# Optimization experiments

Hardware: AMD Instinct MI355X
Metric: run time of the kernel (lower is better)

The kernel has to match this reference:

```python
import jax, jax.numpy as jnp
import numpy as np

EMB = 1024
HID = 2048
HEADS = 16
CONV = 4


def causal_conv1d(z, w):
    # z: [B, H, T], w: [H, K] depthwise causal conv
    K = w.shape[1]
    T = z.shape[-1]
    zp = jnp.pad(z, ((0, 0), (0, 0), (K - 1, 0)))  # [B, H, T+K-1]
    out = jnp.zeros_like(z)
    for k in range(K):  # tiny fixed loop over taps (K<=4)
        out = out + w[None, :, k, None] * jax.lax.dynamic_slice_in_dim(zp, k, T, axis=2)
    return out


def linear_scan(a, b):
    # h_t = a_t * h_{t-1} + b_t along last axis; associative scan
    def combine(c1, c2):
        a1, b1 = c1
        a2, b2 = c2
        return a1 * a2, a2 * b1 + b2
    _, h = jax.lax.associative_scan(combine, (a, b), axis=-1)
    return h


def setup_inputs() -> dict:
    key = jax.random.key(0)
    k1, k2, k3, k4 = jax.random.split(key, 4)
    x = jax.random.normal(k1, (4, 2048, EMB), dtype=jnp.float32)
    w1 = jax.random.normal(k2, (3 * HID, EMB), dtype=jnp.float32) * (EMB ** -0.5)
    w2 = jax.random.normal(k3, (EMB, HID), dtype=jnp.float32) * (HID ** -0.5)
    conv_weight = jax.random.normal(k4, (HID, CONV), dtype=jnp.float32) * (CONV ** -0.5)
    return {"x": x, "w1": w1, "w2": w2, "conv_weight": conv_weight}


def reference(x, w1, w2, conv_weight):
    bsz, seq_len, _ = x.shape
    head_dim = HID // HEADS
    y = jnp.einsum("bse,he->bsh", x, w1)  # [B, S, 3*HID]
    out1, z, h = jnp.split(y, 3, axis=-1)
    z = jnp.swapaxes(z, 1, 2)  # [B, HID, S]
    h = jnp.swapaxes(h, 1, 2)
    z = causal_conv1d(z, conv_weight)
    z = jax.nn.sigmoid(z)
    z = z.reshape(bsz * HEADS, head_dim, seq_len)
    h = h.reshape(bsz * HEADS, head_dim, seq_len)
    h = linear_scan(1.0 - z, z * h)
    out2 = jnp.swapaxes(h.reshape(bsz, HID, seq_len), 1, 2)  # [B, S, HID]
    out = jax.nn.silu(out1) * out2
    return jnp.einsum("bsh,eh->bse", out, w2)
```

## Files before the change

### kernel.cpp

```cpp
#include <hip/hip_runtime.h>
#include <cstdint>

#define EMB 1024
#define HID 2048
#define BATCH 4
#define SEQ 2048
#define MROWS (BATCH * SEQ)
#define N1 (3 * HID)
#define K1 EMB
#define N2 EMB
#define K2 HID

#define NX (MROWS * EMB)
#define NW1 (N1 * K1)
#define NW2 (N2 * K2)

#define SEG 64
#define SLEN (SEQ / SEG)

typedef unsigned short ushort_t;
typedef __bf16 bf16x8 __attribute__((ext_vector_type(8)));
typedef float f32x4 __attribute__((ext_vector_type(4)));
typedef ushort_t us4 __attribute__((ext_vector_type(4)));

__device__ __forceinline__ ushort_t f2bf(float f) {
    uint32_t u = __builtin_bit_cast(uint32_t, f);
    u += 0x7fffu + ((u >> 16) & 1u);
    return (ushort_t)(u >> 16);
}
__device__ __forceinline__ float bf2f(ushort_t h) {
    uint32_t u = ((uint32_t)h) << 16;
    return __builtin_bit_cast(float, u);
}
__device__ __forceinline__ float bflo(uint32_t v) {
    return __builtin_bit_cast(float, v << 16);
}
__device__ __forceinline__ float bfhi(uint32_t v) {
    return __builtin_bit_cast(float, v & 0xffff0000u);
}
__device__ __forceinline__ float sigm(float x) {
    return 1.f / (1.f + __expf(-x));
}

__device__ __forceinline__ void gload_lds16(const ushort_t* g, const ushort_t* l) {
    __builtin_amdgcn_global_load_lds(
        (const __attribute__((address_space(1))) void*)(uintptr_t)(g),
        (__attribute__((address_space(3))) void*)(uint32_t)(uintptr_t)(l),
        16, 0, 0);
}

__global__ __launch_bounds__(256) void cvt_kernel(
    const float* __restrict__ x, const float* __restrict__ w1,
    const float* __restrict__ w2, ushort_t* __restrict__ xb,
    ushort_t* __restrict__ w1b, ushort_t* __restrict__ w2b) {
    const int i = (blockIdx.x * 256 + threadIdx.x) * 4;
    const float* s;
    ushort_t* d;
    if (i < NX) {
        s = x + i; d = xb + i;
    } else if (i < NX + NW1) {
        s = w1 + (i - NX); d = w1b + (i - NX);
    } else {
        s = w2 + (i - NX - NW1); d = w2b + (i - NX - NW1);
    }
    const float4 v = *(const float4*)s;
    us4 o;
    o.x = f2bf(v.x); o.y = f2bf(v.y); o.z = f2bf(v.z); o.w = f2bf(v.w);
    *(us4*)d = o;
}

__device__ __forceinline__ void lda4(bf16x8 (&af)[2][4], const ushort_t* c,
                                     int arow, int quad, int sw) {
#pragma unroll
    for (int s = 0; s < 2; ++s)
#pragma unroll
        for (int i = 0; i < 4; ++i)
            af[s][i] = *(const bf16x8*)&c[(arow + i * 16) * 64 +
                                          (((s * 4 + quad) ^ sw) << 3)];
}
__device__ __forceinline__ void ldb2(bf16x8 (&bfr)[2][2], const ushort_t* c,
                                     int bcol, int quad, int sw) {
#pragma unroll
    for (int s = 0; s < 2; ++s)
#pragma unroll
        for (int j = 0; j < 2; ++j)
            bfr[s][j] = *(const bf16x8*)&c[(bcol + j * 16) * 64 +
                                           (((s * 4 + quad) ^ sw) << 3)];
}
template <int QM, int QN>
__device__ __forceinline__ void mm16(f32x4 (&acc)[8][4],
                                     const bf16x8 (&af)[2][4],
                                     const bf16x8 (&bfr)[2][2]) {
#pragma unroll
    for (int s = 0; s < 2; ++s)
#pragma unroll
        for (int i = 0; i < 4; ++i)
#pragma unroll
            for (int j = 0; j < 2; ++j)
                acc[QM * 4 + i][QN * 2 + j] =
                    __builtin_amdgcn_mfma_f32_16x16x32_bf16(
                        af[s][i], bfr[s][j], acc[QM * 4 + i][QN * 2 + j], 0, 0, 0);
}

template <bool OUT_BF16>
__global__ __launch_bounds__(512, 2) void gemm256(
    const ushort_t* __restrict__ A, const ushort_t* __restrict__ B,
    void* __restrict__ Cv, int M, int N, int K) {
    __shared__ __align__(16) ushort_t sA[2][2][8192];
    __shared__ __align__(16) ushort_t sB[2][2][8192];

    const int tid  = threadIdx.x;
    const int lane = tid & 63;
    const int wave = tid >> 6;
    const int wm   = wave >> 2;
    const int wn   = wave & 3;
    const int quad = lane >> 4;
    const int l15  = lane & 15;
    const int sw   = lane & 7;

    int wg = blockIdx.x;
    const int nwg = gridDim.x;
    if ((nwg & 7) == 0) wg = (wg & 7) * (nwg >> 3) + (wg >> 3);
    const int nbx = N >> 8;
    const int bx = wg % nbx;
    const int by = wg / nbx;
    const long tm0 = (long)by << 8;
    const long tn0 = (long)bx << 8;

    const ushort_t* gA = A + (size_t)tm0 * K;
    const ushort_t* gB = B + (size_t)tn0 * K;

    const int l8 = lane >> 3;
    const int ss = (lane & 7) ^ l8;
    const uint32_t rA = (uint32_t)((wave & 3) * 16 + l8 + (wave >> 2) * 128);
    const int cB = wave * 16 + l8;
    const uint32_t rB = (uint32_t)((cB >> 5) * 64 + (cB & 31));
    const uint32_t offA0 = rA * (uint32_t)K + (uint32_t)ss * 8u;
    const uint32_t offA1 = offA0 + 8u * (uint32_t)K;
    const uint32_t offB0 = rB * (uint32_t)K + (uint32_t)ss * 8u;
    const uint32_t offB1 = offB0 + 8u * (uint32_t)K;

    const auto stA = [&](int tt, int q) {
        ushort_t* d = &sA[tt & 1][q][wave << 10];
        const size_t ko = (size_t)tt * 64 + (size_t)q * 64 * (size_t)K;
        gload_lds16(gA + ko + offA0, d);
        gload_lds16(gA + ko + offA1, d + 512);
    };
    const auto stB = [&](int tt, int q) {
        ushort_t* d = &sB[tt & 1][q][wave << 10];
        const size_t ko = (size_t)tt * 64 + (size_t)q * 32 * (size_t)K;
        gload_lds16(gB + ko + offB0, d);
        gload_lds16(gB + ko + offB1, d + 512);
    };

    const int arow = wm * 64 + l15;
    const int bcol = wn * 32 + l15;

    f32x4 acc[8][4] = {};
    bf16x8 af0[2][4], af1[2][4], bf0[2][2], bf1[2][2];

    const int NT = K >> 6;

    stA(0, 0); stB(0, 0); stB(0, 1); stA(0, 1);
    asm volatile("s_waitcnt vmcnt(0)" ::: "memory");
    __builtin_amdgcn_s_barrier();

    for (int T = 0; T < NT; ++T) {
        const int cur = T & 1;
        const ushort_t* a0 = &sA[cur][0][0];
        const ushort_t* a1 = &sA[cur][1][0];
        const ushort_t* b0 = &sB[cur][0][0];
        const ushort_t* b1 = &sB[cur][1][0];
        const bool st1 = (T + 1 < NT);

        lda4(af0, a0, arow, quad, sw);
        ldb2(bf0, b0, bcol, quad, sw);
        ldb2(bf1, b1, bcol, quad, sw);
        lda4(af1, a1, arow, quad, sw);
        if (st1) {
            stA(T + 1, 0); stB(T + 1, 0);
            stB(T + 1, 1); stA(T + 1, 1);
        }
        __builtin_amdgcn_s_setprio(1);
        mm16<0, 0>(acc, af0, bf0);
        mm16<0, 1>(acc, af0, bf1);
        mm16<1, 0>(acc, af1, bf0);
        mm16<1, 1>(acc, af1, bf1);
        __builtin_amdgcn_s_setprio(0);
        if (st1) asm volatile("s_waitcnt vmcnt(0)" ::: "memory");
        __builtin_amdgcn_s_barrier();
    }

#pragma unroll
    for (int ai = 0; ai < 8; ++ai) {
        const long row0 = tm0 + wm * 128 + (ai >> 2) * 64 + (ai & 3) * 16 + quad * 4;
#pragma unroll
        for (int bj = 0; bj < 4; ++bj) {
            const long col = tn0 + wn * 64 + (bj >> 1) * 32 + (bj & 1) * 16 + l15;
#pragma unroll
            for (int r = 0; r < 4; ++r) {
                if constexpr (OUT_BF16) {
                    ((ushort_t*)Cv)[(size_t)(row0 + r) * N + col] = f2bf(acc[ai][bj][r]);
                } else {
                    ((float*)Cv)[(size_t)(row0 + r) * N + col] = acc[ai][bj][r];
                }
            }
        }
    }
}

__global__ __launch_bounds__(512, 1) void gemm_mn(
    const ushort_t* __restrict__ A, const ushort_t* __restrict__ B,
    float* __restrict__ C, int M, int N, int K) {
    __shared__ __align__(16) ushort_t sA[3][2][8192];
    __shared__ __align__(16) ushort_t sB[3][8192];

    const int tid  = threadIdx.x;
    const int lane = tid & 63;
    const int wave = tid >> 6;
    const int wm   = wave >> 1;
    const int wn   = wave & 1;
    const int quad = lane >> 4;
    const int l15  = lane & 15;
    const int sw   = lane & 7;

    int wg = blockIdx.x;
    const int nwg = gridDim.x;
    if ((nwg & 7) == 0) wg = (wg & 7) * (nwg >> 3) + (wg >> 3);
    const int nbx = N >> 7;
    const int bx = wg % nbx;
    const int by = wg / nbx;
    const long tm0 = (long)by << 8;
    const long tn0 = (long)bx << 7;

    const ushort_t* gA = A + (size_t)tm0 * K;
    const ushort_t* gB = B + (size_t)tn0 * K;

    const int l8 = lane >> 3;
    const int ss = (lane & 7) ^ l8;
    const uint32_t rA = (uint32_t)((wave & 3) * 16 + l8 + (wave >> 2) * 128);
    const uint32_t rB = (uint32_t)(wave * 16 + l8);
    const uint32_t offA0 = rA * (uint32_t)K + (uint32_t)ss * 8u;
    const uint32_t offA1 = offA0 + 8u * (uint32_t)K;
    const uint32_t offB0 = rB * (uint32_t)K + (uint32_t)ss * 8u;
    const uint32_t offB1 = offB0 + 8u * (uint32_t)K;

    const auto stA = [&](int tt, int q) {
        ushort_t* d = &sA[tt % 3][q][wave << 10];
        const size_t ko = (size_t)tt * 64 + (size_t)q * 64 * (size_t)K;
        gload_lds16(gA + ko + offA0, d);
        gload_lds16(gA + ko + offA1, d + 512);
    };
    const auto stB = [&](int tt) {
        ushort_t* d = &sB[tt % 3][wave << 10];
        const size_t ko = (size_t)tt * 64;
        gload_lds16(gB + ko + offB0, d);
        gload_lds16(gB + ko + offB1, d + 512);
    };

    const int cq   = wm & 1;
    const int arow = (wm >> 1) * 64 + l15;
    const int bcol = wn * 64 + l15;

    f32x4 acc[4][4] = {};
    bf16x8 af[2][4], bf[2][4];

    const int NT = K >> 6;

    stA(0, 0); stA(0, 1); stB(0);
    stA(1, 0); stA(1, 1); stB(1);
    asm volatile("s_waitcnt vmcnt(6)" ::: "memory");
    __builtin_amdgcn_s_barrier();

    for (int T = 0; T < NT; ++T) {
        const int cur = T % 3;
        const ushort_t* pa = &sA[cur][cq][0];
        const ushort_t* pb = &sB[cur][0];
        const bool st2 = (T + 2 < NT);

        lda4(af, pa, arow, quad, sw);
        lda4(bf, pb, bcol, quad, sw);
        if (st2) { stA(T + 2, 0); stA(T + 2, 1); stB(T + 2); }
        __builtin_amdgcn_s_setprio(1);
#pragma unroll
        for (int s = 0; s < 2; ++s)
#pragma unroll
            for (int i = 0; i < 4; ++i)
#pragma unroll
                for (int j = 0; j < 4; ++j)
                    acc[i][j] = __builtin_amdgcn_mfma_f32_16x16x32_bf16(
                        af[s][i], bf[s][j], acc[i][j], 0, 0, 0);
        __builtin_amdgcn_s_setprio(0);
        if (st2)                asm volatile("s_waitcnt vmcnt(6)" ::: "memory");
        else if (T + 1 < NT)    asm volatile("s_waitcnt vmcnt(0)" ::: "memory");
        __builtin_amdgcn_s_barrier();
    }

#pragma unroll
    for (int i = 0; i < 4; ++i) {
        const long row0 = tm0 + wm * 64 + i * 16 + quad * 4;
#pragma unroll
        for (int j = 0; j < 4; ++j) {
            const long col = tn0 + wn * 64 + j * 16 + l15;
#pragma unroll
            for (int r = 0; r < 4; ++r)
                C[(size_t)(row0 + r) * N + col] = acc[i][j][r];
        }
    }
}

__global__ __launch_bounds__(256) void scan_part1(
    const ushort_t* __restrict__ y, const float* __restrict__ cw,
    float* __restrict__ Ag, float* __restrict__ Bg) {
    const int gid = blockIdx.x * 256 + threadIdx.x;
    const int ch  = (gid & 1023) * 2;
    const int bs  = gid >> 10;
    const int b   = bs >> 6;
    const int seg = bs & 63;
    const int t0  = seg * SLEN;
    const size_t rowbase = (size_t)b * SEQ;
    const ushort_t* yz = y + 2048 + ch;
    const ushort_t* yh = y + 4096 + ch;

    float w[2][4];
#pragma unroll
    for (int c = 0; c < 2; ++c)
#pragma unroll
        for (int k = 0; k < 4; ++k) w[c][k] = cw[(ch + c) * 4 + k];

    auto ld2 = [&](const ushort_t* p, int t) -> uint32_t {
        return *(const uint32_t*)(p + (rowbase + (size_t)t) * 6144);
    };
    auto zpair = [&](int t, float* out) {
        if (t < 0) { out[0] = 0.f; out[1] = 0.f; }
        else { uint32_t v = ld2(yz, t); out[0] = bflo(v); out[1] = bfhi(v); }
    };

    float z1[2], z2[2], z3[2], A[2] = {1.f, 1.f}, Bv[2] = {0.f, 0.f};
    zpair(t0 - 1, z1); zpair(t0 - 2, z2); zpair(t0 - 3, z3);

#pragma unroll 8
    for (int t = t0; t < t0 + SLEN; ++t) {
        const uint32_t vz = ld2(yz, t);
        const uint32_t vh = ld2(yh, t);
        const float zr[2] = {bflo(vz), bfhi(vz)};
        const float hr[2] = {bflo(vh), bfhi(vh)};
#pragma unroll
        for (int c = 0; c < 2; ++c) {
            const float cv = w[c][0] * z3[c] + w[c][1] * z2[c] +
                             w[c][2] * z1[c] + w[c][3] * zr[c];
            const float s = sigm(cv);
            z3[c] = z2[c]; z2[c] = z1[c]; z1[c] = zr[c];
            const float a = 1.f - s;
            A[c] *= a;
            Bv[c] = a * Bv[c] + s * hr[c];
        }
    }
    const size_t idx = ((size_t)b * SEG + seg) * HID + ch;
    *(float2*)&Ag[idx] = make_float2(A[0], A[1]);
    *(float2*)&Bg[idx] = make_float2(Bv[0], Bv[1]);
}

__global__ __launch_bounds__(256) void scan_part2(
    const float* __restrict__ Ag, const float* __restrict__ Bg,
    float* __restrict__ Cr) {
    const int gid = blockIdx.x * 256 + threadIdx.x;
    const int b  = gid >> 11;
    const int ch = gid & 2047;
    float carry = 0.f;
#pragma unroll
    for (int s = 0; s < SEG; ++s) {
        const size_t idx = ((size_t)b * SEG + s) * HID + ch;
        Cr[idx] = carry;
        carry = Ag[idx] * carry + Bg[idx];
    }
}

__global__ __launch_bounds__(256) void scan_part3(
    const ushort_t* __restrict__ y, const float* __restrict__ cw,
    const float* __restrict__ Cr, ushort_t* __restrict__ u) {
    const int gid = blockIdx.x * 256 + threadIdx.x;
    const int ch  = (gid & 1023) * 2;
    const int bs  = gid >> 10;
    const int b   = bs >> 6;
    const int seg = bs & 63;
    const int t0  = seg * SLEN;
    const size_t rowbase = (size_t)b * SEQ;
    const ushort_t* yo = y + ch;
    const ushort_t* yz = y + 2048 + ch;
    const ushort_t* yh = y + 4096 + ch;

    float w[2][4];
#pragma unroll
    for (int c = 0; c < 2; ++c)
#pragma unroll
        for (int k = 0; k < 4; ++k) w[c][k] = cw[(ch + c) * 4 + k];

    auto ld2 = [&](const ushort_t* p, int t) -> uint32_t {
        return *(const uint32_t*)(p + (rowbase + (size_t)t) * 6144);
    };
    auto zpair = [&](int t, float* out) {
        if (t < 0) { out[0] = 0.f; out[1] = 0.f; }
        else { uint32_t v = ld2(yz, t); out[0] = bflo(v); out[1] = bfhi(v); }
    };

    const size_t cidx = ((size_t)b * SEG + seg) * HID + ch;
    float h[2] = {Cr[cidx], Cr[cidx + 1]};
    float z1[2], z2[2], z3[2];
    zpair(t0 - 1, z1); zpair(t0 - 2, z2); zpair(t0 - 3, z3);

#pragma unroll 8
    for (int t = t0; t < t0 + SLEN; ++t) {
        const uint32_t vz = ld2(yz, t);
        const uint32_t vh = ld2(yh, t);
        const uint32_t vo = ld2(yo, t);
        const float zr[2] = {bflo(vz), bfhi(vz)};
        const float hr[2] = {bflo(vh), bfhi(vh)};
        const float o1[2] = {bflo(vo), bfhi(vo)};
        ushort_t res[2];
#pragma unroll
        for (int c = 0; c < 2; ++c) {
            const float cv = w[c][0] * z3[c] + w[c][1] * z2[c] +
                             w[c][2] * z1[c] + w[c][3] * zr[c];
            const float s = sigm(cv);
            z3[c] = z2[c]; z2[c] = z1[c]; z1[c] = zr[c];
            h[c] = (1.f - s) * h[c] + s * hr[c];
            const float sil = o1[c] * sigm(o1[c]);
            res[c] = f2bf(sil * h[c]);
        }
        *(uint32_t*)&u[(rowbase + (size_t)t) * (size_t)HID + ch] =
            (uint32_t)res[0] | ((uint32_t)res[1] << 16);
    }
}

extern "C" void kernel_launch(void* const* d_in, const int* in_sizes, int n_in,
                              void* d_out, int out_size, void* d_ws, size_t ws_size,
                              hipStream_t stream) {
    const float* x  = (const float*)d_in[0];
    const float* w1 = (const float*)d_in[1];
    const float* w2 = (const float*)d_in[2];
    const float* cw = (const float*)d_in[3];
    char* ws = (char*)d_ws;

    ushort_t* xb  = (ushort_t*)(ws);
    ushort_t* w1b = (ushort_t*)(ws + (size_t)16777216);
    ushort_t* w2b = (ushort_t*)(ws + (size_t)29360128);
    ushort_t* y   = (ushort_t*)(ws + (size_t)33554432);
    ushort_t* u   = (ushort_t*)(ws + (size_t)134217728);
    float* Ag = (float*)(ws);
    float* Bg = (float*)(ws + (size_t)2097152);
    float* Cr = (float*)(ws + (size_t)4194304);
    float* out = (float*)d_out;

    cvt_kernel<<<16384, 256, 0, stream>>>(x, w1, w2, xb, w1b, w2b);
    gemm256<true><<<dim3(768), 512, 0, stream>>>(xb, w1b, (void*)y, MROWS, N1, K1);
    scan_part1<<<1024, 256, 0, stream>>>(y, cw, Ag, Bg);
    scan_part2<<<32, 256, 0, stream>>>(Ag, Bg, Cr);
    scan_part3<<<1024, 256, 0, stream>>>(y, cw, Cr, u);
    gemm_mn<<<dim3(256), 512, 0, stream>>>(u, w2b, out, MROWS, N2, K2);
}
```

Before: 289.1 us.

## Restructure gemm256 into 4-stage K=32 pipeline with register double-buffered fragments

Rewrites the gemm256 main loop to use 32-wide K tiles staged through a 4-deep LDS ring, with global loads issued three tiles ahead and partial vmcnt waits instead of draining all outstanding loads each iteration. LDS fragment reads for the next tile are interleaved between the two halves of the current tile's MFMAs, using ping-pong register sets. The LDS layout and swizzle are changed to match the new staging pattern. This is meant to hide global and LDS latency better, but it doubles the number of barriers per unit of K and raises register pressure under the 2-blocks-per-CU launch bound.

After: 295.5 us. +2.2%, slower.

```diff
diff --git a/kernel.cpp b/kernel.cpp
--- a/kernel.cpp
+++ b/kernel.cpp
@@ -69,45 +69,12 @@
     *(us4*)d = o;
 }
 
-__device__ __forceinline__ void lda4(bf16x8 (&af)[2][4], const ushort_t* c,
-                                     int arow, int quad, int sw) {
-#pragma unroll
-    for (int s = 0; s < 2; ++s)
-#pragma unroll
-        for (int i = 0; i < 4; ++i)
-            af[s][i] = *(const bf16x8*)&c[(arow + i * 16) * 64 +
-                                          (((s * 4 + quad) ^ sw) << 3)];
-}
-__device__ __forceinline__ void ldb2(bf16x8 (&bfr)[2][2], const ushort_t* c,
-                                     int bcol, int quad, int sw) {
-#pragma unroll
-    for (int s = 0; s < 2; ++s)
-#pragma unroll
-        for (int j = 0; j < 2; ++j)
-            bfr[s][j] = *(const bf16x8*)&c[(bcol + j * 16) * 64 +
-                                           (((s * 4 + quad) ^ sw) << 3)];
-}
-template <int QM, int QN>
-__device__ __forceinline__ void mm16(f32x4 (&acc)[8][4],
-                                     const bf16x8 (&af)[2][4],
-                                     const bf16x8 (&bfr)[2][2]) {
-#pragma unroll
-    for (int s = 0; s < 2; ++s)
-#pragma unroll
-        for (int i = 0; i < 4; ++i)
-#pragma unroll
-            for (int j = 0; j < 2; ++j)
-                acc[QM * 4 + i][QN * 2 + j] =
-                    __builtin_amdgcn_mfma_f32_16x16x32_bf16(
-                        af[s][i], bfr[s][j], acc[QM * 4 + i][QN * 2 + j], 0, 0, 0);
-}
-
 template <bool OUT_BF16>
 __global__ __launch_bounds__(512, 2) void gemm256(
     const ushort_t* __restrict__ A, const ushort_t* __restrict__ B,
     void* __restrict__ Cv, int M, int N, int K) {
-    __shared__ __align__(16) ushort_t sA[2][2][8192];
-    __shared__ __align__(16) ushort_t sB[2][2][8192];
+    __shared__ __align__(16) ushort_t sA[4][2][4096];
+    __shared__ __align__(16) ushort_t sB[4][2][4096];
 
     const int tid  = threadIdx.x;
     const int lane = tid & 63;
@@ -116,7 +83,6 @@
     const int wn   = wave & 3;
     const int quad = lane >> 4;
     const int l15  = lane & 15;
-    const int sw   = lane & 7;
 
     int wg = blockIdx.x;
     const int nwg = gridDim.x;
@@ -130,83 +96,120 @@
     const ushort_t* gA = A + (size_t)tm0 * K;
     const ushort_t* gB = B + (size_t)tn0 * K;
 
-    const int l8 = lane >> 3;
-    const int ss = (lane & 7) ^ l8;
-    const uint32_t rA = (uint32_t)((wave & 3) * 16 + l8 + (wave >> 2) * 128);
-    const int cB = wave * 16 + l8;
-    const uint32_t rB = (uint32_t)((cB >> 5) * 64 + (cB & 31));
-    const uint32_t offA0 = rA * (uint32_t)K + (uint32_t)ss * 8u;
-    const uint32_t offA1 = offA0 + 8u * (uint32_t)K;
-    const uint32_t offB0 = rB * (uint32_t)K + (uint32_t)ss * 8u;
-    const uint32_t offB1 = offB0 + 8u * (uint32_t)K;
-
-    const auto stA = [&](int tt, int q) {
-        ushort_t* d = &sA[tt & 1][q][wave << 10];
-        const size_t ko = (size_t)tt * 64 + (size_t)q * 64 * (size_t)K;
-        gload_lds16(gA + ko + offA0, d);
-        gload_lds16(gA + ko + offA1, d + 512);
-    };
-    const auto stB = [&](int tt, int q) {
-        ushort_t* d = &sB[tt & 1][q][wave << 10];
-        const size_t ko = (size_t)tt * 64 + (size_t)q * 32 * (size_t)K;
-        gload_lds16(gB + ko + offB0, d);
-        gload_lds16(gB + ko + offB1, d + 512);
-    };
-
-    const int arow = wm * 64 + l15;
-    const int bcol = wn * 32 + l15;
+    const int l8g = lane >> 3;
+    const int l7g = lane & 7;
+    const int s8  = l7g ^ l8g;
+    const int mloc = (l8g << 1) + (s8 >> 2);
+    const uint32_t soff = (uint32_t)(wave * 16 + mloc) * (uint32_t)K +
+                          (uint32_t)((s8 & 3) << 3);
+
+    const auto STG = [&](int tt) {
+        const int ib = tt & 3;
+        const size_t ko = (size_t)tt * 32;
+        gload_lds16(gA + ko + soff, &sA[ib][0][wave << 9]);
+        gload_lds16(gA + ko + (size_t)128 * K + soff, &sA[ib][1][wave << 9]);
+        gload_lds16(gB + ko + soff, &sB[ib][0][wave << 9]);
+        gload_lds16(gB + ko + (size_t)128 * K + soff, &sB[ib][1][wave << 9]);
+    };
+
+    const int stored = ((((l15 & 1) << 2) + quad) ^ ((l15 >> 1) & 7));
+    const int abase  = (l15 >> 1) * 64 + stored * 8;
+    const int bbase  = ((wn & 1) << 11) + abase;
 
     f32x4 acc[8][4] = {};
-    bf16x8 af0[2][4], af1[2][4], bf0[2][2], bf1[2][2];
-
-    const int NT = K >> 6;
-
-    stA(0, 0); stB(0, 0); stB(0, 1); stA(0, 1);
-    asm volatile("s_waitcnt vmcnt(0)" ::: "memory");
+    bf16x8 aX[8], bX[4], aY[8], bY[4];
+
+    const int NT = K >> 5;
+
+    STG(0); STG(1); STG(2);
+    asm volatile("s_waitcnt vmcnt(4)" ::: "memory");
     __builtin_amdgcn_s_barrier();
 
-    for (int T = 0; T < NT; ++T) {
-        const int cur = T & 1;
-        const ushort_t* a0 = &sA[cur][0][0];
-        const ushort_t* a1 = &sA[cur][1][0];
-        const ushort_t* b0 = &sB[cur][0][0];
-        const ushort_t* b1 = &sB[cur][1][0];
-        const bool st1 = (T + 1 < NT);
-
-        lda4(af0, a0, arow, quad, sw);
-        ldb2(bf0, b0, bcol, quad, sw);
-        ldb2(bf1, b1, bcol, quad, sw);
-        lda4(af1, a1, arow, quad, sw);
-        if (st1) {
-            stA(T + 1, 0); stB(T + 1, 0);
-            stB(T + 1, 1); stA(T + 1, 1);
+    {
+        const ushort_t* pa = &sA[0][wm][0];
+        const ushort_t* pb = &sB[0][wn >> 1][0];
+#pragma unroll
+        for (int i = 0; i < 8; ++i) aX[i] = *(const bf16x8*)&pa[abase + i * 512];
+#pragma unroll
+        for (int j = 0; j < 4; ++j) bX[j] = *(const bf16x8*)&pb[bbase + j * 512];
+    }
+
+    const auto body = [&](int T, bf16x8 (&ac)[8], bf16x8 (&bc)[4],
+                                 bf16x8 (&an)[8], bf16x8 (&bn)[4]) {
+        const int ibn = (T + 1) & 3;
+        const ushort_t* pa = &sA[ibn][wm][0];
+        const ushort_t* pb = &sB[ibn][wn >> 1][0];
+        const bool rd = (T + 1 < NT);
+        const bool st = (T + 3 < NT);
+        if (rd) {
+#pragma unroll
+            for (int i = 0; i < 4; ++i)
+                an[i] = *(const bf16x8*)&pa[abase + i * 512];
         }
         __builtin_amdgcn_s_setprio(1);
-        mm16<0, 0>(acc, af0, bf0);
-        mm16<0, 1>(acc, af0, bf1);
-        mm16<1, 0>(acc, af1, bf0);
-        mm16<1, 1>(acc, af1, bf1);
+#pragma unroll
+        for (int i = 0; i < 4; ++i)
+#pragma unroll
+            for (int j = 0; j < 4; ++j)
+                acc[i][j] = __builtin_amdgcn_mfma_f32_16x16x32_bf16(
+                    ac[i], bc[j], acc[i][j], 0, 0, 0);
         __builtin_amdgcn_s_setprio(0);
-        if (st1) asm volatile("s_waitcnt vmcnt(0)" ::: "memory");
+        if (rd) {
+#pragma unroll
+            for (int i = 4; i < 8; ++i)
+                an[i] = *(const bf16x8*)&pa[abase + i * 512];
+#pragma unroll
+            for (int j = 0; j < 4; ++j)
+                bn[j] = *(const bf16x8*)&pb[bbase + j * 512];
+        }
+        __builtin_amdgcn_s_setprio(1);
+#pragma unroll
+        for (int i = 4; i < 8; ++i)
+#pragma unroll
+            for (int j = 0; j < 4; ++j)
+                acc[i][j] = __builtin_amdgcn_mfma_f32_16x16x32_bf16(
+                    ac[i], bc[j], acc[i][j], 0, 0, 0);
+        __builtin_amdgcn_s_setprio(0);
+        if (st) {
+            STG(T + 3);
+            asm volatile("s_waitcnt vmcnt(4)" ::: "memory");
+        } else {
+            asm volatile("s_waitcnt vmcnt(0)" ::: "memory");
+        }
         __builtin_amdgcn_s_barrier();
-    }
-
-#pragma unroll
-    for (int ai = 0; ai < 8; ++ai) {
-        const long row0 = tm0 + wm * 128 + (ai >> 2) * 64 + (ai & 3) * 16 + quad * 4;
-#pragma unroll
-        for (int bj = 0; bj < 4; ++bj) {
-            const long col = tn0 + wn * 64 + (bj >> 1) * 32 + (bj & 1) * 16 + l15;
+    };
+
+    for (int T = 0; T < NT; T += 2) {
+        body(T, aX, bX, aY, bY);
+        body(T + 1, aY, bY, aX, bX);
+    }
+
+#pragma unroll
+    for (int i = 0; i < 8; ++i) {
+        const long row0 = tm0 + wm * 128 + i * 16 + quad * 4;
+#pragma unroll
+        for (int j = 0; j < 4; ++j) {
+            const long col = tn0 + wn * 64 + j * 16 + l15;
 #pragma unroll
             for (int r = 0; r < 4; ++r) {
                 if constexpr (OUT_BF16) {
-                    ((ushort_t*)Cv)[(size_t)(row0 + r) * N + col] = f2bf(acc[ai][bj][r]);
+                    ((ushort_t*)Cv)[(size_t)(row0 + r) * N + col] = f2bf(acc[i][j][r]);
                 } else {
-                    ((float*)Cv)[(size_t)(row0 + r) * N + col] = acc[ai][bj][r];
+                    ((float*)Cv)[(size_t)(row0 + r) * N + col] = acc[i][j][r];
                 }
             }
         }
     }
+}
+
+__device__ __forceinline__ void lda4(bf16x8 (&af)[2][4], const ushort_t* c,
+                                     int arow, int quad, int sw) {
+#pragma unroll
+    for (int s = 0; s < 2; ++s)
+#pragma unroll
+        for (int i = 0; i < 4; ++i)
+            af[s][i] = *(const bf16x8*)&c[(arow + i * 16) * 64 +
+                                          (((s * 4 + quad) ^ sw) << 3)];
 }
 
 __global__ __launch_bounds__(512, 1) void gemm_mn(
```

## Replace 256x128 second GEMM with 128x128 tile, double buffering, two blocks per CU

Applied to the files above, without the earlier changes.

The second GEMM moves from a 256x128 output tile with 512 threads and triple-buffered LDS to a 128x128 tile with 256 threads, double buffering and two workgroups per CU. The grid grows from 256 to 512 blocks, so the 256 CUs get more blocks and more waves to hide latency. In exchange the prefetch depth drops from two tiles to one, and each block has less data reuse, which raises global and L2 traffic per output.

After: 305.5 us. 5.7% more time.

```diff
diff --git a/kernel.cpp b/kernel.cpp
--- a/kernel.cpp
+++ b/kernel.cpp
@@ -209,11 +209,11 @@
     }
 }
 
-__global__ __launch_bounds__(512, 1) void gemm_mn(
+__global__ __launch_bounds__(256, 2) void gemm128(
     const ushort_t* __restrict__ A, const ushort_t* __restrict__ B,
     float* __restrict__ C, int M, int N, int K) {
-    __shared__ __align__(16) ushort_t sA[3][2][8192];
-    __shared__ __align__(16) ushort_t sB[3][8192];
+    __shared__ __align__(16) ushort_t sA[2][8192];
+    __shared__ __align__(16) ushort_t sB[2][8192];
 
     const int tid  = threadIdx.x;
     const int lane = tid & 63;
@@ -230,36 +230,32 @@
     const int nbx = N >> 7;
     const int bx = wg % nbx;
     const int by = wg / nbx;
-    const long tm0 = (long)by << 8;
+    const long tm0 = (long)by << 7;
     const long tn0 = (long)bx << 7;
 
     const ushort_t* gA = A + (size_t)tm0 * K;
     const ushort_t* gB = B + (size_t)tn0 * K;
 
     const int l8 = lane >> 3;
-    const int ss = (lane & 7) ^ l8;
-    const uint32_t rA = (uint32_t)((wave & 3) * 16 + l8 + (wave >> 2) * 128);
-    const uint32_t rB = (uint32_t)(wave * 16 + l8);
-    const uint32_t offA0 = rA * (uint32_t)K + (uint32_t)ss * 8u;
-    const uint32_t offA1 = offA0 + 8u * (uint32_t)K;
-    const uint32_t offB0 = rB * (uint32_t)K + (uint32_t)ss * 8u;
-    const uint32_t offB1 = offB0 + 8u * (uint32_t)K;
-
-    const auto stA = [&](int tt, int q) {
-        ushort_t* d = &sA[tt % 3][q][wave << 10];
-        const size_t ko = (size_t)tt * 64 + (size_t)q * 64 * (size_t)K;
-        gload_lds16(gA + ko + offA0, d);
-        gload_lds16(gA + ko + offA1, d + 512);
-    };
-    const auto stB = [&](int tt) {
-        ushort_t* d = &sB[tt % 3][wave << 10];
+    const int l7 = lane & 7;
+    const int ss = l7 ^ l8;
+    uint32_t offs[4];
+#pragma unroll
+    for (int i = 0; i < 4; ++i)
+        offs[i] = (uint32_t)((wave * 4 + i) * 8 + l8) * (uint32_t)K +
+                  (uint32_t)(ss << 3);
+
+    const auto stage = [&](int tt) {
+        const int ib = tt & 1;
         const size_t ko = (size_t)tt * 64;
-        gload_lds16(gB + ko + offB0, d);
-        gload_lds16(gB + ko + offB1, d + 512);
-    };
-
-    const int cq   = wm & 1;
-    const int arow = (wm >> 1) * 64 + l15;
+#pragma unroll
+        for (int i = 0; i < 4; ++i) {
+            gload_lds16(gA + ko + offs[i], &sA[ib][(wave * 4 + i) << 9]);
+            gload_lds16(gB + ko + offs[i], &sB[ib][(wave * 4 + i) << 9]);
+        }
+    };
+
+    const int arow = wm * 64 + l15;
     const int bcol = wn * 64 + l15;
 
     f32x4 acc[4][4] = {};
@@ -267,20 +263,19 @@
 
     const int NT = K >> 6;
 
-    stA(0, 0); stA(0, 1); stB(0);
-    stA(1, 0); stA(1, 1); stB(1);
-    asm volatile("s_waitcnt vmcnt(6)" ::: "memory");
+    stage(0);
+    asm volatile("s_waitcnt vmcnt(0)" ::: "memory");
     __builtin_amdgcn_s_barrier();
 
     for (int T = 0; T < NT; ++T) {
-        const int cur = T % 3;
-        const ushort_t* pa = &sA[cur][cq][0];
+        const int cur = T & 1;
+        const ushort_t* pa = &sA[cur][0];
         const ushort_t* pb = &sB[cur][0];
-        const bool st2 = (T + 2 < NT);
+        const bool st1 = (T + 1 < NT);
 
         lda4(af, pa, arow, quad, sw);
         lda4(bf, pb, bcol, quad, sw);
-        if (st2) { stA(T + 2, 0); stA(T + 2, 1); stB(T + 2); }
+        if (st1) stage(T + 1);
         __builtin_amdgcn_s_setprio(1);
 #pragma unroll
         for (int s = 0; s < 2; ++s)
@@ -291,8 +286,7 @@
                     acc[i][j] = __builtin_amdgcn_mfma_f32_16x16x32_bf16(
                         af[s][i], bf[s][j], acc[i][j], 0, 0, 0);
         __builtin_amdgcn_s_setprio(0);
-        if (st2)                asm volatile("s_waitcnt vmcnt(6)" ::: "memory");
-        else if (T + 1 < NT)    asm volatile("s_waitcnt vmcnt(0)" ::: "memory");
+        if (st1) asm volatile("s_waitcnt vmcnt(0)" ::: "memory");
         __builtin_amdgcn_s_barrier();
     }
 
@@ -457,5 +451,5 @@
     scan_part1<<<1024, 256, 0, stream>>>(y, cw, Ag, Bg);
     scan_part2<<<32, 256, 0, stream>>>(Ag, Bg, Cr);
     scan_part3<<<1024, 256, 0, stream>>>(y, cw, Cr, u);
-    gemm_mn<<<dim3(256), 512, 0, stream>>>(u, w2b, out, MROWS, N2, K2);
-}
+    gemm128<<<dim3(512), 256, 0, stream>>>(u, w2b, out, MROWS, N2, K2);
+}
```
